# Performance work log

Hardware: AMD Instinct MI355X
Metric: run time of the kernel (lower is better)

Reference implementation:

```python
import jax, jax.numpy as jnp
import numpy as np

C = 64   # input_channels
H = 128  # hidden_channels


def setup_inputs() -> dict:
    key = jax.random.key(0)
    ks = jax.random.split(key, 13)
    s = lambda k, shape, fan_in: jax.random.uniform(k, shape, jnp.float32, -1.0, 1.0) / np.sqrt(fan_in)
    return {
        "x": jax.random.normal(ks[0], (2, 512, C), jnp.float32),
        "Wa": s(ks[1], (C, H), C),  "ba": s(ks[2], (H,), C),
        "Wb": s(ks[3], (H, H), H), "bb": s(ks[4], (H,), H),
        "Wc1": s(ks[5], (H, H), H), "bc1": s(ks[6], (H,), H),
        "Wc2": s(ks[7], (H, H), H), "bc2": s(ks[8], (H,), H),
        "Wc3": s(ks[9], (H, H), H), "bc3": s(ks[10], (H,), H),
        "Wo": s(ks[11], (H, 1), H), "bo": s(ks[12], (1,), H),
    }


def reference(x, Wa, ba, Wb, bb, Wc1, bc1, Wc2, bc2, Wc3, bc3, Wo, bo):
    B, N, _ = x.shape
    # node MLP
    h = jax.nn.relu(jnp.einsum("bnc,ch->bnh", x, Wa) + ba)
    h = jax.nn.relu(jnp.einsum("bnh,hk->bnk", h, Wb) + bb)
    # pairwise difference: diff[b,i,j] = h[b,j] - h[b,i]  (matches x_a - x_b)
    d = h[:, None, :, :] - h[:, :, None, :]  # [B,N,N,H]
    e = jax.nn.relu(jnp.einsum("bijh,hk->bijk", d, Wc1) + bc1)
    e = jax.nn.relu(jnp.einsum("bijh,hk->bijk", e, Wc2) + bc2)
    e = jax.nn.relu(jnp.einsum("bijh,hk->bijk", e, Wc3) + bc3)
    out = jnp.einsum("bijh,ho->bijo", e, Wo) + bo  # [B,N,N,1]
    return out[..., 0]  # [B,N,N]
```

## Files before the change

### kernel.cpp

```cpp
#include <hip/hip_runtime.h>


typedef _Float16 half_t;
typedef __attribute__((ext_vector_type(2))) _Float16 f16x2;
typedef __attribute__((ext_vector_type(8))) _Float16 f16x8;
typedef __attribute__((ext_vector_type(4))) float f32x4;


__global__ __launch_bounds__(256) void prep_kernel(
    const float* __restrict__ x, const float* __restrict__ Wa, const float* __restrict__ ba,
    const float* __restrict__ Wb, const float* __restrict__ bb, const float* __restrict__ Wc1,
    const float* __restrict__ bc1, const float* __restrict__ Wc2, const float* __restrict__ Wc3,
    half_t* __restrict__ gh, half_t* __restrict__ gbh,
    half_t* __restrict__ W2T, half_t* __restrict__ W3T)
{
  const int t = threadIdx.x;
  if (blockIdx.x >= 256) {
    const int bid = blockIdx.x - 256;
    const int layer = bid >> 3, nt = bid & 7;
    const int ks = t >> 6, L = t & 63, q = L >> 4, cc = L & 15;
    const float* src = layer ? Wc3 : Wc2;
    half_t* dst = layer ? W3T : W2T;
    f16x8 v;
    #pragma unroll
    for (int e = 0; e < 8; e++)
      v[e] = (half_t)src[(32 * ks + 8 * q + e) * 128 + 16 * nt + cc];
    *(f16x8*)(dst + (nt * 4 + ks) * 512 + L * 8) = v;
    return;
  }
  __shared__ float sx[64 * 6];
  __shared__ float sh1[128 * 6];
  __shared__ float sh2[128 * 6];
  const int n0 = blockIdx.x * 4;
  const int col = t & 127, hf = t >> 7;

  sx[(t & 63) * 6 + (t >> 6)] = x[(n0 + (t >> 6)) * 64 + (t & 63)];
  __syncthreads();

  float a0 = ba[col], a1 = a0;
  #pragma unroll
  for (int cc = 0; cc < 64; cc++) {
    const float wv = Wa[cc * 128 + col];
    const float2 xv = *(const float2*)(sx + cc * 6 + hf * 2);
    a0 = fmaf(xv.x, wv, a0); a1 = fmaf(xv.y, wv, a1);
  }
  *(float2*)(sh1 + col * 6 + hf * 2) = make_float2(fmaxf(a0, 0.f), fmaxf(a1, 0.f));
  __syncthreads();

  float b0 = bb[col], b1 = b0;
  #pragma unroll
  for (int k = 0; k < 128; k++) {
    const float wv = Wb[k * 128 + col];
    const float2 hv = *(const float2*)(sh1 + k * 6 + hf * 2);
    b0 = fmaf(hv.x, wv, b0); b1 = fmaf(hv.y, wv, b1);
  }
  *(float2*)(sh2 + col * 6 + hf * 2) = make_float2(fmaxf(b0, 0.f), fmaxf(b1, 0.f));
  __syncthreads();

  float c0 = 0.f, c1 = 0.f;
  #pragma unroll
  for (int k = 0; k < 128; k++) {
    const float wv = Wc1[k * 128 + col];
    const float2 hv = *(const float2*)(sh2 + k * 6 + hf * 2);
    c0 = fmaf(hv.x, wv, c0); c1 = fmaf(hv.y, wv, c1);
  }
  const float bv = bc1[col];
  const int r0 = n0 + hf * 2;
  gh [(r0 + 0) * 128 + col] = (half_t)c0;
  gh [(r0 + 1) * 128 + col] = (half_t)c1;
  gbh[(r0 + 0) * 128 + col] = (half_t)(c0 + bv);
  gbh[(r0 + 1) * 128 + col] = (half_t)(c1 + bv);
}

static __device__ inline f16x8 relu_sub8(f16x8 a, f16x8 b) {
  f16x8 d = a - b;
  const f16x8 z = {};
  return __builtin_elementwise_max(d, z);
}

__global__ __launch_bounds__(512, 2)
void edge_kernel(
    const half_t* __restrict__ gh, const half_t* __restrict__ gbh,
    const half_t* __restrict__ W2T, const half_t* __restrict__ W3T,
    const float* __restrict__ bc2, const float* __restrict__ bc3,
    const float* __restrict__ Wo, const float* __restrict__ bo,
    float* __restrict__ out)
{
  __shared__ __align__(16) half_t sW2[16384];
  __shared__ __align__(16) half_t sW3[16384];
  __shared__ __align__(16) float  sBf[384];
  __shared__ __align__(16) half_t sE[8 * 4096];

  const int t = threadIdx.x, lane = t & 63, w = t >> 6;
  const int c = lane & 15, q = lane >> 4;
  const int bid = blockIdx.x;
  const int b = bid >> 8, jh = (bid >> 7) & 1, ic = bid & 127;
  const int i0 = ic * 4;
  const int j0w = jh * 256 + w * 32;

  #pragma unroll
  for (int k = 0; k < 4; k++) {
    const int off = (k * 512 + t) * 8;
    *(f16x8*)(sW2 + off) = *(const f16x8*)(W2T + off);
    *(f16x8*)(sW3 + off) = *(const f16x8*)(W3T + off);
  }
  if (t < 384) sBf[t] = (t < 128) ? bc2[t] : ((t < 256) ? bc3[t - 128] : Wo[t - 256]);
  __syncthreads();

  half_t* sEw = sE + w * 4096;
  const float bo0 = bo[0];
  const int packoff = ((q >> 1) * 16 + c) * 8 + (q & 1) * 4;
  const int rdoff = lane * 8;

  f16x8 gj[4][2];
  #pragma unroll
  for (int ks = 0; ks < 4; ks++)
    #pragma unroll
    for (int jt = 0; jt < 2; jt++)
      gj[ks][jt] = *(const f16x8*)(gbh + (size_t)(b * 512 + j0w + jt * 16 + c) * 128 + ks * 32 + q * 8);

  #pragma unroll 1
  for (int u = 0; u < 4; u++) {
    const int i = i0 + u;

    f16x8 e1[4][2];
    {
      f16x8 gih[4];
      #pragma unroll
      for (int ks = 0; ks < 4; ks++)
        gih[ks] = *(const f16x8*)(gh + (size_t)(b * 512 + i) * 128 + ks * 32 + q * 8);
      #pragma unroll
      for (int ks = 0; ks < 4; ks++)
        #pragma unroll
        for (int jt = 0; jt < 2; jt++)
          e1[ks][jt] = relu_sub8(gj[ks][jt], gih[ks]);
    }

    #pragma unroll
    for (int nt = 0; nt < 8; nt++) {
      f16x8 wf[4];
      #pragma unroll
      for (int ks = 0; ks < 4; ks++)
        wf[ks] = *(const f16x8*)(sW2 + nt * 2048 + ks * 512 + rdoff);
      const f32x4 b2 = *(const f32x4*)(sBf + nt * 16 + q * 4);
      f32x4 acc[2] = {b2, b2};
      __builtin_amdgcn_s_setprio(1);
      #pragma unroll
      for (int ks = 0; ks < 4; ks++)
        #pragma unroll
        for (int jt = 0; jt < 2; jt++)
          acc[jt] = __builtin_amdgcn_mfma_f32_16x16x32_f16(wf[ks], e1[ks][jt], acc[jt], 0, 0, 0);
      __builtin_amdgcn_s_setprio(0);
      const int po = ((nt >> 1) * 512) + packoff + (nt & 1) * 256;
      #pragma unroll
      for (int jt = 0; jt < 2; jt++) {
        const f32x4 v = acc[jt];
        f16x2 h01, h23;
        h01[0] = (half_t)fmaxf(v[0], 0.f); h01[1] = (half_t)fmaxf(v[1], 0.f);
        h23[0] = (half_t)fmaxf(v[2], 0.f); h23[1] = (half_t)fmaxf(v[3], 0.f);
        uint2 uv;
        uv.x = __builtin_bit_cast(unsigned int, h01);
        uv.y = __builtin_bit_cast(unsigned int, h23);
        *(uint2*)(sEw + jt * 2048 + po) = uv;
      }
    }

    f16x8 be[4][2];
    #pragma unroll
    for (int ks3 = 0; ks3 < 4; ks3++)
      #pragma unroll
      for (int jt = 0; jt < 2; jt++)
        be[ks3][jt] = *(const f16x8*)(sEw + (jt * 4 + ks3) * 512 + rdoff);

    float p[2] = {0.f, 0.f};
    #pragma unroll
    for (int nt = 0; nt < 8; nt++) {
      f16x8 wf[4];
      #pragma unroll
      for (int ks3 = 0; ks3 < 4; ks3++)
        wf[ks3] = *(const f16x8*)(sW3 + nt * 2048 + ks3 * 512 + rdoff);
      const f32x4 b3 = *(const f32x4*)(sBf + 128 + nt * 16 + q * 4);
      f32x4 acc[2] = {b3, b3};
      __builtin_amdgcn_s_setprio(1);
      #pragma unroll
      for (int ks3 = 0; ks3 < 4; ks3++)
        #pragma unroll
        for (int jt = 0; jt < 2; jt++)
          acc[jt] = __builtin_amdgcn_mfma_f32_16x16x32_f16(wf[ks3], be[ks3][jt], acc[jt], 0, 0, 0);
      __builtin_amdgcn_s_setprio(0);
      const f32x4 wo = *(const f32x4*)(sBf + 256 + nt * 16 + q * 4);
      #pragma unroll
      for (int jt = 0; jt < 2; jt++)
        #pragma unroll
        for (int r = 0; r < 4; r++)
          p[jt] = fmaf(fmaxf(acc[jt][r], 0.f), wo[r], p[jt]);
    }

    #pragma unroll
    for (int jt = 0; jt < 2; jt++) {
      p[jt] += __shfl_xor(p[jt], 16, 64);
      p[jt] += __shfl_xor(p[jt], 32, 64);
    }
    if (q == 0) {
      const size_t base = ((size_t)(b * 512 + i)) * 512 + j0w;
      #pragma unroll
      for (int jt = 0; jt < 2; jt++)
        out[base + jt * 16 + c] = p[jt] + bo0;
    }
  }
}

extern "C" void kernel_launch(void* const* d_in, const int* in_sizes, int n_in,
                              void* d_out, int out_size, void* d_ws, size_t ws_size,
                              hipStream_t stream)
{
  const float* x   = (const float*)d_in[0];
  const float* Wa  = (const float*)d_in[1];
  const float* ba  = (const float*)d_in[2];
  const float* Wb  = (const float*)d_in[3];
  const float* bb  = (const float*)d_in[4];
  const float* Wc1 = (const float*)d_in[5];
  const float* bc1 = (const float*)d_in[6];
  const float* Wc2 = (const float*)d_in[7];
  const float* bc2 = (const float*)d_in[8];
  const float* Wc3 = (const float*)d_in[9];
  const float* bc3 = (const float*)d_in[10];
  const float* Wo  = (const float*)d_in[11];
  const float* bo  = (const float*)d_in[12];
  float* out = (float*)d_out;

  char* ws = (char*)d_ws;
  half_t* gh  = (half_t*)ws;
  half_t* gbh = (half_t*)(ws + 262144);
  half_t* W2T = (half_t*)(ws + 524288);
  half_t* W3T = (half_t*)(ws + 557056);

  prep_kernel<<<272, 256, 0, stream>>>(x, Wa, ba, Wb, bb, Wc1, bc1, Wc2, Wc3,
                                       gh, gbh, W2T, W3T);
  edge_kernel<<<512, 512, 0, stream>>>(gh, gbh, W2T, W3T, bc2, bc3, Wo, bo, out);
}
```

Before: 118.7 us.

## Split edge kernel into producer/consumer warps with register-resident W3

The edge kernel now has two warp roles. Four warps compute layer 2 into double-buffered shared tiles, and four warps compute layer 3 plus the output projection from the previous step. W3 fragments are held in registers by the consumer warps instead of being read from shared memory, and each block handles 16 i rows over 128 j columns, giving 256 blocks. The aim is to overlap the two GEMM stages and cut shared-memory traffic for W3. The costs are a block-wide barrier every step, much higher register pressure from 32 fragment registers, and only 256 blocks, which may underfill the 256 CUs at 2 blocks per CU. gbh is also reloaded from global memory on every step.

```diff
diff --git a/kernel.cpp b/kernel.cpp
--- a/kernel.cpp
+++ b/kernel.cpp
@@ -87,126 +87,132 @@
     float* __restrict__ out)
 {
   __shared__ __align__(16) half_t sW2[16384];
-  __shared__ __align__(16) half_t sW3[16384];
   __shared__ __align__(16) float  sBf[384];
-  __shared__ __align__(16) half_t sE[8 * 4096];
+  __shared__ __align__(16) half_t sE[4 * 2 * 4096];
 
   const int t = threadIdx.x, lane = t & 63, w = t >> 6;
   const int c = lane & 15, q = lane >> 4;
   const int bid = blockIdx.x;
-  const int b = bid >> 8, jh = (bid >> 7) & 1, ic = bid & 127;
-  const int i0 = ic * 4;
-  const int j0w = jh * 256 + w * 32;
+  const int b = bid >> 7, jq = (bid >> 5) & 3, ic = bid & 31;
+  const int i0 = ic * 16;
+  const bool producer = (w < 4);
+  const int pw = producer ? w : (w - 4);
+  const int j0w = jq * 128 + pw * 32;
 
   #pragma unroll
   for (int k = 0; k < 4; k++) {
     const int off = (k * 512 + t) * 8;
     *(f16x8*)(sW2 + off) = *(const f16x8*)(W2T + off);
-    *(f16x8*)(sW3 + off) = *(const f16x8*)(W3T + off);
   }
   if (t < 384) sBf[t] = (t < 128) ? bc2[t] : ((t < 256) ? bc3[t - 128] : Wo[t - 256]);
-  __syncthreads();
-
-  half_t* sEw = sE + w * 4096;
+
   const float bo0 = bo[0];
   const int packoff = ((q >> 1) * 16 + c) * 8 + (q & 1) * 4;
   const int rdoff = lane * 8;
 
-  f16x8 gj[4][2];
-  #pragma unroll
-  for (int ks = 0; ks < 4; ks++)
+  f16x8 w3[8][4];
+  if (!producer) {
     #pragma unroll
-    for (int jt = 0; jt < 2; jt++)
-      gj[ks][jt] = *(const f16x8*)(gbh + (size_t)(b * 512 + j0w + jt * 16 + c) * 128 + ks * 32 + q * 8);
-
-  #pragma unroll 1
-  for (int u = 0; u < 4; u++) {
-    const int i = i0 + u;
-
-    f16x8 e1[4][2];
-    {
-      f16x8 gih[4];
+    for (int nt = 0; nt < 8; nt++)
       #pragma unroll
       for (int ks = 0; ks < 4; ks++)
-        gih[ks] = *(const f16x8*)(gh + (size_t)(b * 512 + i) * 128 + ks * 32 + q * 8);
-      #pragma unroll
-      for (int ks = 0; ks < 4; ks++)
-        #pragma unroll
-        for (int jt = 0; jt < 2; jt++)
-          e1[ks][jt] = relu_sub8(gj[ks][jt], gih[ks]);
-    }
-
-    #pragma unroll
-    for (int nt = 0; nt < 8; nt++) {
-      f16x8 wf[4];
-      #pragma unroll
-      for (int ks = 0; ks < 4; ks++)
-        wf[ks] = *(const f16x8*)(sW2 + nt * 2048 + ks * 512 + rdoff);
-      const f32x4 b2 = *(const f32x4*)(sBf + nt * 16 + q * 4);
-      f32x4 acc[2] = {b2, b2};
-      __builtin_amdgcn_s_setprio(1);
-      #pragma unroll
-      for (int ks = 0; ks < 4; ks++)
-        #pragma unroll
-        for (int jt = 0; jt < 2; jt++)
-          acc[jt] = __builtin_amdgcn_mfma_f32_16x16x32_f16(wf[ks], e1[ks][jt], acc[jt], 0, 0, 0);
-      __builtin_amdgcn_s_setprio(0);
-      const int po = ((nt >> 1) * 512) + packoff + (nt & 1) * 256;
-      #pragma unroll
-      for (int jt = 0; jt < 2; jt++) {
-        const f32x4 v = acc[jt];
-        f16x2 h01, h23;
-        h01[0] = (half_t)fmaxf(v[0], 0.f); h01[1] = (half_t)fmaxf(v[1], 0.f);
-        h23[0] = (half_t)fmaxf(v[2], 0.f); h23[1] = (half_t)fmaxf(v[3], 0.f);
-        uint2 uv;
-        uv.x = __builtin_bit_cast(unsigned int, h01);
-        uv.y = __builtin_bit_cast(unsigned int, h23);
-        *(uint2*)(sEw + jt * 2048 + po) = uv;
+        w3[nt][ks] = *(const f16x8*)(W3T + (nt * 4 + ks) * 512 + rdoff);
+  }
+  __syncthreads();
+
+  #pragma unroll 1
+  for (int step = 0; step < 17; ++step) {
+    if (producer) {
+      if (step < 16) {
+        const int i = i0 + step;
+        f16x8 e1[4][2];
+        {
+          f16x8 gih[4];
+          #pragma unroll
+          for (int ks = 0; ks < 4; ks++)
+            gih[ks] = *(const f16x8*)(gh + (size_t)(b * 512 + i) * 128 + ks * 32 + q * 8);
+          #pragma unroll
+          for (int ks = 0; ks < 4; ks++)
+            #pragma unroll
+            for (int jt = 0; jt < 2; jt++) {
+              const f16x8 gj = *(const f16x8*)(gbh + (size_t)(b * 512 + j0w + jt * 16 + c) * 128 + ks * 32 + q * 8);
+              e1[ks][jt] = relu_sub8(gj, gih[ks]);
+            }
+        }
+        half_t* sEw = sE + (pw * 2 + (step & 1)) * 4096;
+        #pragma unroll
+        for (int nt = 0; nt < 8; nt++) {
+          f16x8 wf[4];
+          #pragma unroll
+          for (int ks = 0; ks < 4; ks++)
+            wf[ks] = *(const f16x8*)(sW2 + nt * 2048 + ks * 512 + rdoff);
+          const f32x4 b2 = *(const f32x4*)(sBf + nt * 16 + q * 4);
+          f32x4 acc[2] = {b2, b2};
+          __builtin_amdgcn_s_setprio(1);
+          #pragma unroll
+          for (int ks = 0; ks < 4; ks++)
+            #pragma unroll
+            for (int jt = 0; jt < 2; jt++)
+              acc[jt] = __builtin_amdgcn_mfma_f32_16x16x32_f16(wf[ks], e1[ks][jt], acc[jt], 0, 0, 0);
+          __builtin_amdgcn_s_setprio(0);
+          const int po = ((nt >> 1) * 512) + packoff + (nt & 1) * 256;
+          #pragma unroll
+          for (int jt = 0; jt < 2; jt++) {
+            const f32x4 v = acc[jt];
+            f16x2 h01, h23;
+            h01[0] = (half_t)fmaxf(v[0], 0.f); h01[1] = (half_t)fmaxf(v[1], 0.f);
+            h23[0] = (half_t)fmaxf(v[2], 0.f); h23[1] = (half_t)fmaxf(v[3], 0.f);
+            uint2 uv;
+            uv.x = __builtin_bit_cast(unsigned int, h01);
+            uv.y = __builtin_bit_cast(unsigned int, h23);
+            *(uint2*)(sEw + jt * 2048 + po) = uv;
+          }
+        }
+      }
+    } else {
+      if (step >= 1) {
+        const int i = i0 + step - 1;
+        const half_t* sEc = sE + (pw * 2 + ((step - 1) & 1)) * 4096;
+        f16x8 be[4][2];
+        #pragma unroll
+        for (int ks3 = 0; ks3 < 4; ks3++)
+          #pragma unroll
+          for (int jt = 0; jt < 2; jt++)
+            be[ks3][jt] = *(const f16x8*)(sEc + (jt * 4 + ks3) * 512 + rdoff);
+
+        float p[2] = {0.f, 0.f};
+        #pragma unroll
+        for (int nt = 0; nt < 8; nt++) {
+          const f32x4 b3 = *(const f32x4*)(sBf + 128 + nt * 16 + q * 4);
+          f32x4 acc[2] = {b3, b3};
+          __builtin_amdgcn_s_setprio(1);
+          #pragma unroll
+          for (int ks3 = 0; ks3 < 4; ks3++)
+            #pragma unroll
+            for (int jt = 0; jt < 2; jt++)
+              acc[jt] = __builtin_amdgcn_mfma_f32_16x16x32_f16(w3[nt][ks3], be[ks3][jt], acc[jt], 0, 0, 0);
+          __builtin_amdgcn_s_setprio(0);
+          const f32x4 wo = *(const f32x4*)(sBf + 256 + nt * 16 + q * 4);
+          #pragma unroll
+          for (int jt = 0; jt < 2; jt++)
+            #pragma unroll
+            for (int r = 0; r < 4; r++)
+              p[jt] = fmaf(fmaxf(acc[jt][r], 0.f), wo[r], p[jt]);
+        }
+        #pragma unroll
+        for (int jt = 0; jt < 2; jt++) {
+          p[jt] += __shfl_xor(p[jt], 16, 64);
+          p[jt] += __shfl_xor(p[jt], 32, 64);
+        }
+        if (q == 0) {
+          const size_t base = ((size_t)(b * 512 + i)) * 512 + j0w;
+          #pragma unroll
+          for (int jt = 0; jt < 2; jt++)
+            out[base + jt * 16 + c] = p[jt] + bo0;
+        }
       }
     }
-
-    f16x8 be[4][2];
-    #pragma unroll
-    for (int ks3 = 0; ks3 < 4; ks3++)
-      #pragma unroll
-      for (int jt = 0; jt < 2; jt++)
-        be[ks3][jt] = *(const f16x8*)(sEw + (jt * 4 + ks3) * 512 + rdoff);
-
-    float p[2] = {0.f, 0.f};
-    #pragma unroll
-    for (int nt = 0; nt < 8; nt++) {
-      f16x8 wf[4];
-      #pragma unroll
-      for (int ks3 = 0; ks3 < 4; ks3++)
-        wf[ks3] = *(const f16x8*)(sW3 + nt * 2048 + ks3 * 512 + rdoff);
-      const f32x4 b3 = *(const f32x4*)(sBf + 128 + nt * 16 + q * 4);
-      f32x4 acc[2] = {b3, b3};
-      __builtin_amdgcn_s_setprio(1);
-      #pragma unroll
-      for (int ks3 = 0; ks3 < 4; ks3++)
-        #pragma unroll
-        for (int jt = 0; jt < 2; jt++)
-          acc[jt] = __builtin_amdgcn_mfma_f32_16x16x32_f16(wf[ks3], be[ks3][jt], acc[jt], 0, 0, 0);
-      __builtin_amdgcn_s_setprio(0);
-      const f32x4 wo = *(const f32x4*)(sBf + 256 + nt * 16 + q * 4);
-      #pragma unroll
-      for (int jt = 0; jt < 2; jt++)
-        #pragma unroll
-        for (int r = 0; r < 4; r++)
-          p[jt] = fmaf(fmaxf(acc[jt][r], 0.f), wo[r], p[jt]);
-    }
-
-    #pragma unroll
-    for (int jt = 0; jt < 2; jt++) {
-      p[jt] += __shfl_xor(p[jt], 16, 64);
-      p[jt] += __shfl_xor(p[jt], 32, 64);
-    }
-    if (q == 0) {
-      const size_t base = ((size_t)(b * 512 + i)) * 512 + j0w;
-      #pragma unroll
-      for (int jt = 0; jt < 2; jt++)
-        out[base + jt * 16 + c] = p[jt] + bo0;
-    }
+    __syncthreads();
   }
 }
 
@@ -237,5 +243,5 @@
 
   prep_kernel<<<272, 256, 0, stream>>>(x, Wa, ba, Wb, bb, Wc1, bc1, Wc2, Wc3,
                                        gh, gbh, W2T, W3T);
-  edge_kernel<<<512, 512, 0, stream>>>(gh, gbh, W2T, W3T, bc2, bc3, Wo, bo, out);
-}
+  edge_kernel<<<256, 512, 0, stream>>>(gh, gbh, W2T, W3T, bc2, bc3, Wo, bo, out);
+}
```

Measured after the change: 131.0 us. +10.3%, slower.

## Switch edge MLP to 32x32x16 MFMA with register shuffle handoff between layers

Applied to the files above, without the earlier changes.

Replaces the 16x16x32 MFMA tiling with 32x32x16 MFMAs and repacks the transposed weights to match. The layer-2 output is rearranged into layer-3 B-operand fragments with cross-half-wave shuffles rather than a round trip through shared memory, which removes the sE buffer. Each block now covers all 512 j values, so the grid is halved to 256 blocks. Per-u gbh loads move inside the loop, and the wider tiles raise register pressure and lower the block count, which may hurt occupancy and load balance across CUs.

```diff
diff --git a/kernel.cpp b/kernel.cpp
--- a/kernel.cpp
+++ b/kernel.cpp
@@ -5,6 +5,7 @@
 typedef __attribute__((ext_vector_type(2))) _Float16 f16x2;
 typedef __attribute__((ext_vector_type(8))) _Float16 f16x8;
 typedef __attribute__((ext_vector_type(4))) float f32x4;
+typedef __attribute__((ext_vector_type(16))) float f32x16;
 
 
 __global__ __launch_bounds__(256) void prep_kernel(
@@ -17,15 +18,19 @@
   const int t = threadIdx.x;
   if (blockIdx.x >= 256) {
     const int bid = blockIdx.x - 256;
-    const int layer = bid >> 3, nt = bid & 7;
-    const int ks = t >> 6, L = t & 63, q = L >> 4, cc = L & 15;
+    const int layer = bid >> 3;
+    const int f = (bid & 7) * 4 + (t >> 6);
+    const int L = t & 63;
+    const int nt32 = f >> 3, kt = f & 7;
+    const int row0 = kt * 16 + 8 * (L >> 5);
+    const int col = nt32 * 32 + (L & 31);
     const float* src = layer ? Wc3 : Wc2;
     half_t* dst = layer ? W3T : W2T;
     f16x8 v;
     #pragma unroll
     for (int e = 0; e < 8; e++)
-      v[e] = (half_t)src[(32 * ks + 8 * q + e) * 128 + 16 * nt + cc];
-    *(f16x8*)(dst + (nt * 4 + ks) * 512 + L * 8) = v;
+      v[e] = (half_t)src[(row0 + e) * 128 + col];
+    *(f16x8*)(dst + f * 512 + L * 8) = v;
     return;
   }
   __shared__ float sx[64 * 6];
@@ -76,6 +81,13 @@
   f16x8 d = a - b;
   const f16x8 z = {};
   return __builtin_elementwise_max(d, z);
+}
+
+static __device__ inline unsigned pack2relu(float a, float b) {
+  f16x2 hx;
+  hx[0] = (half_t)fmaxf(a, 0.f);
+  hx[1] = (half_t)fmaxf(b, 0.f);
+  return __builtin_bit_cast(unsigned, hx);
 }
 
 __global__ __launch_bounds__(512, 2)
@@ -89,14 +101,14 @@
   __shared__ __align__(16) half_t sW2[16384];
   __shared__ __align__(16) half_t sW3[16384];
   __shared__ __align__(16) float  sBf[384];
-  __shared__ __align__(16) half_t sE[8 * 4096];
 
   const int t = threadIdx.x, lane = t & 63, w = t >> 6;
-  const int c = lane & 15, q = lane >> 4;
+  const int h = lane >> 5, c32 = lane & 31;
   const int bid = blockIdx.x;
-  const int b = bid >> 8, jh = (bid >> 7) & 1, ic = bid & 127;
+  const int b = bid >> 7, ic = bid & 127;
   const int i0 = ic * 4;
-  const int j0w = jh * 256 + w * 32;
+  const int j0 = w * 64;
+  const bool hs = (h != 0);
 
   #pragma unroll
   for (int k = 0; k < 4; k++) {
@@ -107,105 +119,108 @@
   if (t < 384) sBf[t] = (t < 128) ? bc2[t] : ((t < 256) ? bc3[t - 128] : Wo[t - 256]);
   __syncthreads();
 
-  half_t* sEw = sE + w * 4096;
   const float bo0 = bo[0];
-  const int packoff = ((q >> 1) * 16 + c) * 8 + (q & 1) * 4;
   const int rdoff = lane * 8;
-
-  f16x8 gj[4][2];
-  #pragma unroll
-  for (int ks = 0; ks < 4; ks++)
-    #pragma unroll
-    for (int jt = 0; jt < 2; jt++)
-      gj[ks][jt] = *(const f16x8*)(gbh + (size_t)(b * 512 + j0w + jt * 16 + c) * 128 + ks * 32 + q * 8);
 
   #pragma unroll 1
   for (int u = 0; u < 4; u++) {
     const int i = i0 + u;
 
-    f16x8 e1[4][2];
+    f16x8 e1[2][8];
     {
-      f16x8 gih[4];
-      #pragma unroll
-      for (int ks = 0; ks < 4; ks++)
-        gih[ks] = *(const f16x8*)(gh + (size_t)(b * 512 + i) * 128 + ks * 32 + q * 8);
-      #pragma unroll
-      for (int ks = 0; ks < 4; ks++)
-        #pragma unroll
-        for (int jt = 0; jt < 2; jt++)
-          e1[ks][jt] = relu_sub8(gj[ks][jt], gih[ks]);
-    }
-
-    #pragma unroll
-    for (int nt = 0; nt < 8; nt++) {
-      f16x8 wf[4];
-      #pragma unroll
-      for (int ks = 0; ks < 4; ks++)
-        wf[ks] = *(const f16x8*)(sW2 + nt * 2048 + ks * 512 + rdoff);
-      const f32x4 b2 = *(const f32x4*)(sBf + nt * 16 + q * 4);
-      f32x4 acc[2] = {b2, b2};
-      __builtin_amdgcn_s_setprio(1);
-      #pragma unroll
-      for (int ks = 0; ks < 4; ks++)
-        #pragma unroll
-        for (int jt = 0; jt < 2; jt++)
-          acc[jt] = __builtin_amdgcn_mfma_f32_16x16x32_f16(wf[ks], e1[ks][jt], acc[jt], 0, 0, 0);
-      __builtin_amdgcn_s_setprio(0);
-      const int po = ((nt >> 1) * 512) + packoff + (nt & 1) * 256;
-      #pragma unroll
-      for (int jt = 0; jt < 2; jt++) {
-        const f32x4 v = acc[jt];
-        f16x2 h01, h23;
-        h01[0] = (half_t)fmaxf(v[0], 0.f); h01[1] = (half_t)fmaxf(v[1], 0.f);
-        h23[0] = (half_t)fmaxf(v[2], 0.f); h23[1] = (half_t)fmaxf(v[3], 0.f);
-        uint2 uv;
-        uv.x = __builtin_bit_cast(unsigned int, h01);
-        uv.y = __builtin_bit_cast(unsigned int, h23);
-        *(uint2*)(sEw + jt * 2048 + po) = uv;
-      }
-    }
-
-    f16x8 be[4][2];
-    #pragma unroll
-    for (int ks3 = 0; ks3 < 4; ks3++)
-      #pragma unroll
-      for (int jt = 0; jt < 2; jt++)
-        be[ks3][jt] = *(const f16x8*)(sEw + (jt * 4 + ks3) * 512 + rdoff);
-
-    float p[2] = {0.f, 0.f};
-    #pragma unroll
-    for (int nt = 0; nt < 8; nt++) {
-      f16x8 wf[4];
-      #pragma unroll
-      for (int ks3 = 0; ks3 < 4; ks3++)
-        wf[ks3] = *(const f16x8*)(sW3 + nt * 2048 + ks3 * 512 + rdoff);
-      const f32x4 b3 = *(const f32x4*)(sBf + 128 + nt * 16 + q * 4);
-      f32x4 acc[2] = {b3, b3};
-      __builtin_amdgcn_s_setprio(1);
-      #pragma unroll
-      for (int ks3 = 0; ks3 < 4; ks3++)
-        #pragma unroll
-        for (int jt = 0; jt < 2; jt++)
-          acc[jt] = __builtin_amdgcn_mfma_f32_16x16x32_f16(wf[ks3], be[ks3][jt], acc[jt], 0, 0, 0);
-      __builtin_amdgcn_s_setprio(0);
-      const f32x4 wo = *(const f32x4*)(sBf + 256 + nt * 16 + q * 4);
+      f16x8 gi[8];
+      #pragma unroll
+      for (int kt = 0; kt < 8; kt++)
+        gi[kt] = *(const f16x8*)(gh + (size_t)(b * 512 + i) * 128 + kt * 16 + 8 * h);
       #pragma unroll
       for (int jt = 0; jt < 2; jt++)
         #pragma unroll
-        for (int r = 0; r < 4; r++)
-          p[jt] = fmaf(fmaxf(acc[jt][r], 0.f), wo[r], p[jt]);
-    }
-
+        for (int kt = 0; kt < 8; kt++) {
+          const f16x8 gj = *(const f16x8*)(gbh + (size_t)(b * 512 + j0 + jt * 32 + c32) * 128 + kt * 16 + 8 * h);
+          e1[jt][kt] = relu_sub8(gj, gi[kt]);
+        }
+    }
+
+    f16x8 e2f[2][8];
     #pragma unroll
-    for (int jt = 0; jt < 2; jt++) {
-      p[jt] += __shfl_xor(p[jt], 16, 64);
-      p[jt] += __shfl_xor(p[jt], 32, 64);
-    }
-    if (q == 0) {
-      const size_t base = ((size_t)(b * 512 + i)) * 512 + j0w;
-      #pragma unroll
-      for (int jt = 0; jt < 2; jt++)
-        out[base + jt * 16 + c] = p[jt] + bo0;
+    for (int nt = 0; nt < 4; nt++) {
+      f32x4 b2q[4];
+      #pragma unroll
+      for (int rq = 0; rq < 4; rq++)
+        b2q[rq] = *(const f32x4*)(sBf + nt * 32 + rq * 8 + h * 4);
+      f32x16 acc0, acc1;
+      #pragma unroll
+      for (int r = 0; r < 16; r++) acc0[r] = b2q[r >> 2][r & 3];
+      acc1 = acc0;
+      __builtin_amdgcn_s_setprio(1);
+      #pragma unroll
+      for (int kt = 0; kt < 8; kt++) {
+        const f16x8 wf = *(const f16x8*)(sW2 + (nt * 8 + kt) * 512 + rdoff);
+        acc0 = __builtin_amdgcn_mfma_f32_32x32x16_f16(wf, e1[0][kt], acc0, 0, 0, 0);
+        acc1 = __builtin_amdgcn_mfma_f32_32x32x16_f16(wf, e1[1][kt], acc1, 0, 0, 0);
+      }
+      __builtin_amdgcn_s_setprio(0);
+      #pragma unroll
+      for (int jt = 0; jt < 2; jt++) {
+        const f32x16 a = jt ? acc1 : acc0;
+        {
+          const unsigned u0 = pack2relu(a[0], a[1]),  u1 = pack2relu(a[2], a[3]);
+          const unsigned u2 = pack2relu(a[4], a[5]),  u3 = pack2relu(a[6], a[7]);
+          const unsigned s0 = __shfl_xor(u0, 32, 64), s1 = __shfl_xor(u1, 32, 64);
+          const unsigned s2 = __shfl_xor(u2, 32, 64), s3 = __shfl_xor(u3, 32, 64);
+          uint4 fu;
+          fu.x = hs ? s2 : u0; fu.y = hs ? s3 : u1;
+          fu.z = hs ? u2 : s0; fu.w = hs ? u3 : s1;
+          e2f[jt][2 * nt] = __builtin_bit_cast(f16x8, fu);
+        }
+        {
+          const unsigned u0 = pack2relu(a[8],  a[9]),  u1 = pack2relu(a[10], a[11]);
+          const unsigned u2 = pack2relu(a[12], a[13]), u3 = pack2relu(a[14], a[15]);
+          const unsigned s0 = __shfl_xor(u0, 32, 64), s1 = __shfl_xor(u1, 32, 64);
+          const unsigned s2 = __shfl_xor(u2, 32, 64), s3 = __shfl_xor(u3, 32, 64);
+          uint4 fu;
+          fu.x = hs ? s2 : u0; fu.y = hs ? s3 : u1;
+          fu.z = hs ? u2 : s0; fu.w = hs ? u3 : s1;
+          e2f[jt][2 * nt + 1] = __builtin_bit_cast(f16x8, fu);
+        }
+      }
+    }
+
+    float p0 = 0.f, p1 = 0.f;
+    #pragma unroll
+    for (int mt = 0; mt < 4; mt++) {
+      f32x4 b3q[4], woq[4];
+      #pragma unroll
+      for (int rq = 0; rq < 4; rq++) {
+        b3q[rq] = *(const f32x4*)(sBf + 128 + mt * 32 + rq * 8 + h * 4);
+        woq[rq] = *(const f32x4*)(sBf + 256 + mt * 32 + rq * 8 + h * 4);
+      }
+      f32x16 a0, a1;
+      #pragma unroll
+      for (int r = 0; r < 16; r++) a0[r] = b3q[r >> 2][r & 3];
+      a1 = a0;
+      __builtin_amdgcn_s_setprio(1);
+      #pragma unroll
+      for (int kt = 0; kt < 8; kt++) {
+        const f16x8 wf = *(const f16x8*)(sW3 + (mt * 8 + kt) * 512 + rdoff);
+        a0 = __builtin_amdgcn_mfma_f32_32x32x16_f16(wf, e2f[0][kt], a0, 0, 0, 0);
+        a1 = __builtin_amdgcn_mfma_f32_32x32x16_f16(wf, e2f[1][kt], a1, 0, 0, 0);
+      }
+      __builtin_amdgcn_s_setprio(0);
+      #pragma unroll
+      for (int r = 0; r < 16; r++) {
+        const float wv = woq[r >> 2][r & 3];
+        p0 = fmaf(fmaxf(a0[r], 0.f), wv, p0);
+        p1 = fmaf(fmaxf(a1[r], 0.f), wv, p1);
+      }
+    }
+
+    p0 += __shfl_xor(p0, 32, 64);
+    p1 += __shfl_xor(p1, 32, 64);
+    if (h == 0) {
+      const size_t base = ((size_t)(b * 512 + i)) * 512 + j0;
+      out[base + c32]      = p0 + bo0;
+      out[base + 32 + c32] = p1 + bo0;
     }
   }
 }
@@ -237,5 +252,5 @@
 
   prep_kernel<<<272, 256, 0, stream>>>(x, Wa, ba, Wb, bb, Wc1, bc1, Wc2, Wc3,
                                        gh, gbh, W2T, W3T);
-  edge_kernel<<<512, 512, 0, stream>>>(gh, gbh, W2T, W3T, bc2, bc3, Wo, bo, out);
-}
+  edge_kernel<<<256, 512, 0, stream>>>(gh, gbh, W2T, W3T, bc2, bc3, Wo, bo, out);
+}
```

New measurement: 341.7 us. +187.8%, slower.
